# Kernel tuning notes

Hardware: AMD Instinct MI355X
Metric: run time of the kernel (lower is better)

## Reference

```python
import jax, jax.numpy as jnp
import numpy as np
from jax import lax

B = 4096
IM = 64
HID = 256          # LSTM hidden
OBS_D = 400        # obs embedding dim
SAMP_D = 16        # sample embedding dim
ADDR_D = 16        # address embedding dim
IN_D = OBS_D + SAMP_D + ADDR_D  # 432 LSTM input dim


def setup_inputs() -> dict:
    key = jax.random.key(0)
    ks = jax.random.split(key, 32)
    n = jax.random.normal
    s = 0.05
    return {
        "obs": n(ks[0], (B, IM, IM), jnp.float32),
        "program_id": jax.random.randint(ks[1], (B,), 0, 3),
        "shape_id": jax.random.randint(ks[2], (B,), 0, 2),
        "shape_id_0": jax.random.randint(ks[3], (B,), 0, 2),
        "shape_id_1": jax.random.randint(ks[4], (B,), 0, 2),
        "eps_rp": n(ks[5], (B, 2), jnp.float32),
        "eps_rp0": n(ks[6], (B, 2), jnp.float32),
        "eps_rp1": n(ks[7], (B, 2), jnp.float32),
        # CNN obs embedder (stand-in for util.init_cnn(output_dim=16), flattening to 400)
        "conv1_w": n(ks[8], (32, 1, 3, 3)) * s,
        "conv1_b": n(ks[9], (32,)) * s,
        "conv2_w": n(ks[10], (16, 32, 3, 3)) * s,
        "conv2_b": n(ks[11], (16,)) * s,
        # raw_position_embedder: MLP 2 -> 100 -> 100 -> 16
        "mlp_w1": n(ks[12], (100, 2)) * s,
        "mlp_b1": n(ks[13], (100,)) * s,
        "mlp_w2": n(ks[14], (100, 100)) * s,
        "mlp_b2": n(ks[15], (100,)) * s,
        "mlp_w3": n(ks[16], (SAMP_D, 100)) * s,
        "mlp_b3": n(ks[17], (SAMP_D,)) * s,
        # LSTMCell params (PyTorch layout: [4H, in], gate order i,f,g,o)
        "W_ih": n(ks[18], (4 * HID, IN_D)) * s,
        "b_ih": n(ks[19], (4 * HID,)) * s,
        "W_hh": n(ks[20], (4 * HID, HID)) * s,
        "b_hh": n(ks[21], (4 * HID,)) * s,
        "addr_emb": n(ks[22], (7, ADDR_D)),
        "pid_emb": n(ks[23], (3, SAMP_D)),
        "sid_emb": n(ks[24], (2, SAMP_D)),
        "pid_ext_w": n(ks[25], (3, HID)) * s,
        "pid_ext_b": n(ks[26], (3,)) * s,
        "sid_ext_w": n(ks[27], (2, HID)) * s,
        "sid_ext_b": n(ks[28], (2,)) * s,
        "rp_ext_w": n(ks[29], (4, HID)) * s,
        "rp_ext_b": n(ks[30], (4,)) * s,
    }


def reference(obs, program_id, shape_id, shape_id_0, shape_id_1, eps_rp, eps_rp0, eps_rp1,
              conv1_w, conv1_b, conv2_w, conv2_b,
              mlp_w1, mlp_b1, mlp_w2, mlp_b2, mlp_w3, mlp_b3,
              W_ih, b_ih, W_hh, b_hh,
              addr_emb, pid_emb, sid_emb,
              pid_ext_w, pid_ext_b, sid_ext_w, sid_ext_b, rp_ext_w, rp_ext_b):
    b = obs.shape[0]
    # obs embedder: [B,1,64,64] -> conv s2 -> conv s2 -> avgpool 3x3 -> [B,16,5,5] -> [B,400]
    x = obs[:, None]
    x = jax.nn.relu(lax.conv_general_dilated(x, conv1_w, (2, 2), ((1, 1), (1, 1))) + conv1_b[None, :, None, None])
    x = jax.nn.relu(lax.conv_general_dilated(x, conv2_w, (2, 2), ((1, 1), (1, 1))) + conv2_b[None, :, None, None])
    x = lax.reduce_window(x, 0.0, lax.add, (1, 1, 3, 3), (1, 1, 3, 3), 'VALID') / 9.0
    obs_emb = x.reshape(b, OBS_D)

    def step(samp, aid, h, c):
        a = jnp.broadcast_to(addr_emb[aid], (b, ADDR_D))
        xin = jnp.concatenate([obs_emb, samp, a], axis=-1)
        g = xin @ W_ih.T + b_ih + h @ W_hh.T + b_hh
        i, f, gg, o = jnp.split(g, 4, axis=-1)
        c2 = jax.nn.sigmoid(f) * c + jax.nn.sigmoid(i) * jnp.tanh(gg)
        return jax.nn.sigmoid(o) * jnp.tanh(c2), c2

    zs = jnp.zeros((b, SAMP_D), obs.dtype)
    zh = jnp.zeros((b, HID), obs.dtype)
    h0, c0 = step(zs, 0, zh, zh)
    pid_logits = h0 @ pid_ext_w.T + pid_ext_b
    prev_pid = pid_emb[program_id]

    # branch 0 (program_id == 0): shape_id then raw_position
    h1, c1 = step(prev_pid, 1, h0, c0)
    sid_logits = h1 @ sid_ext_w.T + sid_ext_b
    h2, _ = step(sid_emb[shape_id], 4, h1, c1)
    rp = h2 @ rp_ext_w.T + rp_ext_b
    rp_b0 = rp[:, :2] + jnp.exp(rp[:, 2:]) * eps_rp

    # branch 1 (program_id != 0): shape_id_0, shape_id_1, raw_position_0, raw_position_1
    h1b, c1b = step(prev_pid, 2, h0, c0)
    sid0_logits = h1b @ sid_ext_w.T + sid_ext_b
    h2b, c2b = step(sid_emb[shape_id_0], 3, h1b, c1b)
    sid1_logits = h2b @ sid_ext_w.T + sid_ext_b
    h3b, c3b = step(sid_emb[shape_id_1], 5, h2b, c2b)
    rp0p = h3b @ rp_ext_w.T + rp_ext_b
    rp0 = rp0p[:, :2] + jnp.exp(rp0p[:, 2:]) * eps_rp0
    z = jnp.tanh(rp0 @ mlp_w1.T + mlp_b1)
    z = jnp.tanh(z @ mlp_w2.T + mlp_b2)
    rp0_emb = z @ mlp_w3.T + mlp_b3
    h4b, _ = step(rp0_emb, 6, h3b, c3b)
    rp1p = h4b @ rp_ext_w.T + rp_ext_b
    rp1 = rp1p[:, :2] + jnp.exp(rp1p[:, 2:]) * eps_rp1

    # [B, 3+2+2+2+2+2+2] = [B, 15]
    return jnp.concatenate([pid_logits, sid_logits, rp_b0, sid0_logits, sid1_logits, rp0, rp1], axis=-1)
```

## Files before the change

### kernel.cpp

```cpp
#include <hip/hip_runtime.h>
#include <hip/hip_bf16.h>
#include <math.h>

#define BATCH 4096
#define HID 256
#define OUT_W 15
#define AK 448

typedef unsigned short ushort_t;
typedef unsigned int uint_t;

using bf16x8 = __attribute__((ext_vector_type(8))) short;
using f32x4v = __attribute__((ext_vector_type(4))) float;
using f32x2 = __attribute__((ext_vector_type(2))) float;

__device__ __forceinline__ float sigf(float x) { return 1.0f / (1.0f + __expf(-x)); }
__device__ __forceinline__ float tanh_fast(float x) { return 1.0f - 2.0f / (__expf(2.0f * x) + 1.0f); }
__device__ __forceinline__ float bf2f(ushort_t u) { return __uint_as_float(((uint_t)u) << 16); }
__device__ __forceinline__ ushort_t f2bf(float x) {
    uint_t b = __float_as_uint(x);
    return (ushort_t)((b + 0x7fffu + ((b >> 16) & 1u)) >> 16);
}

__global__ __launch_bounds__(256) void prep_kernel(
    const float* __restrict__ W_ih, const float* __restrict__ W_hh,
    const float* __restrict__ b_ih, const float* __restrict__ b_hh,
    const float* __restrict__ addr_emb, const float* __restrict__ pid_emb,
    const float* __restrict__ sid_emb,
    const float* __restrict__ mlp_w2, const float* __restrict__ mlp_w3,
    const float* __restrict__ conv1_w, const float* __restrict__ conv1_b,
    const float* __restrict__ conv2_w,
    float* __restrict__ W_ih_T, ushort_t* __restrict__ Wb,
    float* __restrict__ bias_all, float* __restrict__ pid_rows,
    float* __restrict__ sid_rows, float* __restrict__ w2t, float* __restrict__ w3t,
    float* __restrict__ w1pp, ushort_t* __restrict__ Btg,
    ushort_t* __restrict__ Wobs_b)
{
    int blk = blockIdx.x, t = threadIdx.x;
    if (blk < 16) {
        __shared__ float tile[64][65];
        int j0 = blk * 64;
        int k0 = 384;
        for (int i = t; i < 4096; i += 256) {
            int r = i >> 6, c = i & 63;
            int k = k0 + c;
            tile[r][c] = (k < 432) ? W_ih[(size_t)(j0 + r) * 432 + k] : 0.f;
        }
        __syncthreads();
        for (int i = t; i < 4096; i += 256) {
            int r = i >> 6, c = i & 63;
            int k = k0 + r;
            if (k < 432) W_ih_T[(size_t)k * 1024 + j0 + c] = tile[c][r];
        }
    } else if (blk == 16) {
        const int aids[7] = {0, 1, 4, 2, 3, 5, 6};
        for (int s = 0; s < 7; s++) {
            int aid = aids[s];
            for (int j = t; j < 1024; j += 256) {
                float v = b_ih[j] + b_hh[j];
                #pragma unroll
                for (int k = 0; k < 16; k++)
                    v += addr_emb[aid * 16 + k] * W_ih[(size_t)j * 432 + 416 + k];
                bias_all[s * 1024 + j] = v;
            }
        }
    } else if (blk == 17) {
        for (int p = 0; p < 3; p++)
            for (int j = t; j < 1024; j += 256) {
                float v = 0.f;
                #pragma unroll
                for (int k = 0; k < 16; k++)
                    v += pid_emb[p * 16 + k] * W_ih[(size_t)j * 432 + 400 + k];
                pid_rows[p * 1024 + j] = v;
            }
        for (int p = 0; p < 2; p++)
            for (int j = t; j < 1024; j += 256) {
                float v = 0.f;
                #pragma unroll
                for (int k = 0; k < 16; k++)
                    v += sid_emb[p * 16 + k] * W_ih[(size_t)j * 432 + 400 + k];
                sid_rows[p * 1024 + j] = v;
            }
    } else if (blk == 18) {
        for (int i = t; i < 10000; i += 256) {
            int o = i / 100, k = i % 100;
            w2t[k * 100 + o] = mlp_w2[i];
        }
        for (int i = t; i < 1600; i += 256) {
            int o = i / 100, k = i % 100;
            w3t[k * 16 + o] = mlp_w3[i];
        }
    } else if (blk == 19) {
        for (int i = t; i < 320; i += 256) {
            int half = i & 1, idx = i >> 1;
            int k = idx % 10, pr = idx / 10;
            int icq = pr >> 2, i2 = pr & 3;
            int ic = icq * 8 + i2 + half * 4;
            w1pp[i] = (k < 9) ? conv1_w[ic * 9 + k] : conv1_b[ic];
        }
        for (int i = t; i < 4608; i += 256) {
            int tap = i >> 9;
            int rem = i & 511;
            int oc = rem >> 5, ic = rem & 31;
            Btg[i] = f2bf(conv2_w[(size_t)(oc * 32 + ic) * 9 + tap]);
        }
    } else if (blk < 36) {
        int seg = blk - 20;
        for (int i = seg * 16384 + t; i < (seg + 1) * 16384; i += 256)
            Wb[i] = f2bf(W_hh[i]);
    } else {
        int col0 = (blk - 36) * 32;
        for (int i = t; i < 32 * AK; i += 256) {
            int c = col0 + i / AK, k = i % AK;
            Wobs_b[(size_t)c * AK + k] = (k < 400) ? f2bf(W_ih[(size_t)c * 432 + k]) : (ushort_t)0;
        }
    }
}

#define CE_RS 640
#define CO_RS 680
#define SM2S 72
#define C2S_CS 324
#define C2S_RS 20
__global__ __launch_bounds__(512, 4) void conv_kernel(
    const float* __restrict__ obs, const float* __restrict__ w1pp,
    const ushort_t* __restrict__ Btg, const float* __restrict__ b2,
    ushort_t* __restrict__ obs_emb_b)
{
    __shared__ __align__(16) ushort_t cE[17 * CE_RS];
    __shared__ __align__(16) ushort_t cO[17 * CO_RS];
    __shared__ __align__(16) float c2s[16 * C2S_CS];
    __shared__ __align__(16) float sm2[33 * SM2S];
    __shared__ __align__(16) float w1s[320];
    const int b = blockIdx.x, t = threadIdx.x;
    const float* og = obs + (size_t)b * 4096;

    const int w = t >> 6, L = t & 63, q = L >> 4, ln = L & 15;

    {
        uint_t* zE = (uint_t*)cE;
        uint_t* zO = (uint_t*)cO;
        for (int i = t; i < CE_RS / 2; i += 512) zE[i] = 0;
        for (int i = t; i < CO_RS / 2; i += 512) zO[i] = 0;
        if (t < 320) {
            int row = (t / 20) + 1, d = t % 20;
            zO[row * (CO_RS / 2) + d] = 0;
        }
    }
    if (t < 80) ((float4*)w1s)[t] = ((const float4*)w1pp)[t];
    if (t < 33) {
        int sw = (t >> 1) & 1;
        sm2[t * SM2S + sw * 4 + 3] = 0.f;
    }

    auto stage_obs = [&](int ph) {
        for (int i = t; i < 33 * 16; i += 512) {
            int row = i >> 4, c4 = i & 15;
            int sw = (row >> 1) & 1;
            int orow = 32 * ph - 1 + row;
            float4 v = float4{0.f, 0.f, 0.f, 0.f};
            if (orow >= 0) v = ((const float4*)(og + (size_t)orow * 64))[c4];
            *(float4*)&sm2[row * SM2S + ((1 + c4) ^ sw) * 4] = v;
        }
    };

    auto conv1_phase = [&](int ph) {
        const int r = t >> 5, g = (t >> 2) & 7, icq = t & 3;
        const int brow = ph ? r : (r + 1);
        float Pt[3][12];
        #pragma unroll
        for (int d = 0; d < 3; d++) {
            int row = 2 * r + d;
            int sw = (row >> 1) & 1;
            const float* base = &sm2[row * SM2S];
            #pragma unroll
            for (int j4 = 0; j4 < 3; j4++) {
                float4 v = *(const float4*)(base + ((2 * g + j4) ^ sw) * 4);
                Pt[d][j4 * 4 + 0] = v.x; Pt[d][j4 * 4 + 1] = v.y;
                Pt[d][j4 * 4 + 2] = v.z; Pt[d][j4 * 4 + 3] = v.w;
            }
        }
        const float* wpbase = &w1s[icq * 80];
        #pragma unroll
        for (int p = 0; p < 4; p++) {
            f32x2 pbc[9];
            #pragma unroll
            for (int d = 0; d < 3; d++)
                #pragma unroll
                for (int dx = 0; dx < 3; dx++) {
                    float v = Pt[d][2 * p + 3 + dx];
                    pbc[d * 3 + dx] = f32x2{v, v};
                }
            f32x2 sall[4];
            #pragma unroll
            for (int i = 0; i < 4; i++) {
                const float* wp = wpbase + i * 20;
                float4 wv0 = *(const float4*)(wp);
                float4 wv1 = *(const float4*)(wp + 4);
                float4 wv2 = *(const float4*)(wp + 8);
                float4 wv3 = *(const float4*)(wp + 12);
                float4 wv4 = *(const float4*)(wp + 16);
                f32x2 W2[10] = {f32x2{wv0.x, wv0.y}, f32x2{wv0.z, wv0.w},
                                f32x2{wv1.x, wv1.y}, f32x2{wv1.z, wv1.w},
                                f32x2{wv2.x, wv2.y}, f32x2{wv2.z, wv2.w},
                                f32x2{wv3.x, wv3.y}, f32x2{wv3.z, wv3.w},
                                f32x2{wv4.x, wv4.y}, f32x2{wv4.z, wv4.w}};
                f32x2 a2 = W2[9];
                #pragma unroll
                for (int k = 0; k < 9; k++)
                    a2 = __builtin_elementwise_fma(pbc[k], W2[k], a2);
                a2 = __builtin_elementwise_max(a2, f32x2{0.f, 0.f});
                sall[i] = a2;
            }
            uint_t d0, d1, d2, d3;
            asm("v_cvt_pk_bf16_f32 %0, %1, %2" : "=v"(d0) : "v"(sall[0].x), "v"(sall[1].x));
            asm("v_cvt_pk_bf16_f32 %0, %1, %2" : "=v"(d1) : "v"(sall[2].x), "v"(sall[3].x));
            asm("v_cvt_pk_bf16_f32 %0, %1, %2" : "=v"(d2) : "v"(sall[0].y), "v"(sall[1].y));
            asm("v_cvt_pk_bf16_f32 %0, %1, %2" : "=v"(d3) : "v"(sall[2].y), "v"(sall[3].y));
            int c = 4 * g + p;
            ushort_t* dst = (c & 1)
                ? &cO[brow * CO_RS + ((c + 1) >> 1) * 40 + icq * 8]
                : &cE[brow * CE_RS + (c >> 1) * 40 + icq * 8];
            *(uint4*)dst = uint4{d0, d1, d2, d3};
        }
    };

    auto conv2_phase = [&](int ph) {
        bf16x8 Bv[9];
        #pragma unroll
        for (int tap = 0; tap < 9; tap++)
            Bv[tap] = *reinterpret_cast<const bf16x8*>(&Btg[(tap * 16 + ln) * 32 + q * 8]);
        const int y = 8 * ph + w;
        f32x4v C = {0.f, 0.f, 0.f, 0.f};
        #pragma unroll
        for (int dy = 0; dy < 3; dy++) {
            int br = 2 * y + dy;
            if (br >= 17) br -= 17;
            bf16x8 a0 = *reinterpret_cast<const bf16x8*>(&cO[br * CO_RS + ln * 40 + q * 8]);
            bf16x8 a1 = *reinterpret_cast<const bf16x8*>(&cE[br * CE_RS + ln * 40 + q * 8]);
            bf16x8 a2 = *reinterpret_cast<const bf16x8*>(&cO[br * CO_RS + (ln + 1) * 40 + q * 8]);
            C = __builtin_amdgcn_mfma_f32_16x16x32_bf16(a0, Bv[dy * 3 + 0], C, 0, 0, 0);
            C = __builtin_amdgcn_mfma_f32_16x16x32_bf16(a1, Bv[dy * 3 + 1], C, 0, 0, 0);
            C = __builtin_amdgcn_mfma_f32_16x16x32_bf16(a2, Bv[dy * 3 + 2], C, 0, 0, 0);
        }
        float bb2 = b2[ln];
        float4 o;
        o.x = fmaxf(C[0] + bb2, 0.f);
        o.y = fmaxf(C[1] + bb2, 0.f);
        o.z = fmaxf(C[2] + bb2, 0.f);
        o.w = fmaxf(C[3] + bb2, 0.f);
        *(float4*)&c2s[ln * C2S_CS + y * C2S_RS + q * 4] = o;
    };

    stage_obs(0);
    __syncthreads();
    conv1_phase(0);
    __syncthreads();
    stage_obs(1);
    conv2_phase(0);
    __syncthreads();
    conv1_phase(1);
    __syncthreads();
    conv2_phase(1);
    __syncthreads();

    ushort_t* ew = (ushort_t*)w1s;
    if (t < 400) {
        int c = t / 25, rem = t % 25, py = rem / 5, px = rem % 5;
        float s = 0.f;
        #pragma unroll
        for (int dy = 0; dy < 3; dy++)
            #pragma unroll
            for (int dx = 0; dx < 3; dx++)
                s += c2s[c * C2S_CS + (3 * py + dy) * C2S_RS + 3 * px + dx];
        ew[t] = f2bf(s * (1.f / 9.f));
    } else if (t < AK) {
        ew[t] = 0;
    }
    __syncthreads();
    if (t < 56)
        ((uint4*)(obs_emb_b + (size_t)b * AK))[t] = ((const uint4*)ew)[t];
}

__global__ __launch_bounds__(256) void obs_gemm(
    const ushort_t* __restrict__ Ab, const ushort_t* __restrict__ Wob,
    ushort_t* __restrict__ outp)
{
    __shared__ __align__(16) ushort_t As[64 * 72];
    __shared__ __align__(16) ushort_t ob[64 * 132];
    const int t = threadIdx.x;
    const int bm = blockIdx.x & 63, bu = blockIdx.x >> 6;
    const int b0 = bm * 64, n0 = bu * 128;
    const int w = t >> 6, L = t & 63, q = L >> 4, ln = L & 15;
    const int m0 = w * 16;

    f32x4v acc[8];
    #pragma unroll
    for (int i = 0; i < 8; i++) acc[i] = f32x4v{0.f, 0.f, 0.f, 0.f};

    for (int kc = 0; kc < 7; kc++) {
        #pragma unroll
        for (int ii = 0; ii < 2; ii++) {
            int i = t + ii * 256;
            int row = i >> 3, c8 = i & 7;
            *(uint4*)&As[row * 72 + c8 * 8] =
                *(const uint4*)&Ab[(size_t)(b0 + row) * AK + kc * 64 + c8 * 8];
        }
        __syncthreads();
        bf16x8 a[2];
        #pragma unroll
        for (int ks = 0; ks < 2; ks++)
            a[ks] = *reinterpret_cast<const bf16x8*>(&As[(m0 + ln) * 72 + ks * 32 + q * 8]);
        #pragma unroll
        for (int ct = 0; ct < 8; ct++) {
            const ushort_t* wr = Wob + (size_t)(n0 + ct * 16 + ln) * AK + kc * 64 + q * 8;
            bf16x8 bv0 = *reinterpret_cast<const bf16x8*>(wr);
            bf16x8 bv1 = *reinterpret_cast<const bf16x8*>(wr + 32);
            acc[ct] = __builtin_amdgcn_mfma_f32_16x16x32_bf16(a[0], bv0, acc[ct], 0, 0, 0);
            acc[ct] = __builtin_amdgcn_mfma_f32_16x16x32_bf16(a[1], bv1, acc[ct], 0, 0, 0);
        }
        __syncthreads();
    }
    #pragma unroll
    for (int ct = 0; ct < 8; ct++)
        #pragma unroll
        for (int j = 0; j < 4; j++)
            ob[(m0 + q * 4 + j) * 132 + ct * 16 + ln] = f2bf(acc[ct][j]);
    __syncthreads();
    #pragma unroll
    for (int p2 = 0; p2 < 4; p2++) {
        int idx = t + p2 * 256;
        int row = idx >> 4, c8 = idx & 15;
        uint4 v = *(const uint4*)&ob[row * 132 + c8 * 8];
        *(uint4*)&outp[(size_t)(b0 + row) * 1024 + n0 + c8 * 8] = v;
    }
}

template <int N>
__device__ __forceinline__ void head_logits_f(
    const ushort_t* hsrc, const float* __restrict__ hw, const float* __restrict__ hb,
    int off, float* red, float* __restrict__ out, int b0, int t)
{
    const int row = t >> 5, seg = t & 31;
    float part[N] = {};
    const ushort_t* hr = hsrc + row * 272 + seg * 8;
    #pragma unroll
    for (int e = 0; e < 8; e++) {
        float hv = bf2f(hr[e]);
        #pragma unroll
        for (int m = 0; m < N; m++) part[m] += hv * hw[m * 256 + seg * 8 + e];
    }
    #pragma unroll
    for (int m = 0; m < N; m++) red[(row * 32 + seg) * 4 + m] = part[m];
    __syncthreads();
    if (t < 16 * N) {
        int r2 = t / N, m = t % N;
        float s = hb[m];
        for (int p = 0; p < 32; p++) s += red[(r2 * 32 + p) * 4 + m];
        out[(size_t)(b0 + r2) * OUT_W + off + m] = s;
    }
    __syncthreads();
}

__device__ __forceinline__ void head_rp_f(
    const ushort_t* hsrc, const float* __restrict__ hw, const float* __restrict__ hb,
    const float* __restrict__ eps, int off, float* red, float* hdr,
    float* __restrict__ out, float* rp0s, int b0, int t)
{
    const int row = t >> 5, seg = t & 31;
    float part[4] = {0.f, 0.f, 0.f, 0.f};
    const ushort_t* hr = hsrc + row * 272 + seg * 8;
    #pragma unroll
    for (int e = 0; e < 8; e++) {
        float hv = bf2f(hr[e]);
        #pragma unroll
        for (int m = 0; m < 4; m++) part[m] += hv * hw[m * 256 + seg * 8 + e];
    }
    #pragma unroll
    for (int m = 0; m < 4; m++) red[(row * 32 + seg) * 4 + m] = part[m];
    __syncthreads();
    if (t < 64) {
        int r2 = t >> 2, m = t & 3;
        float s = hb[m];
        for (int p = 0; p < 32; p++) s += red[(r2 * 32 + p) * 4 + m];
        hdr[t] = s;
    }
    __syncthreads();
    if (t < 16) {
        int R = b0 + t;
        float v0 = hdr[t * 4 + 0] + __expf(hdr[t * 4 + 2]) * eps[(size_t)R * 2 + 0];
        float v1 = hdr[t * 4 + 1] + __expf(hdr[t * 4 + 3]) * eps[(size_t)R * 2 + 1];
        out[(size_t)R * OUT_W + off + 0] = v0;
        out[(size_t)R * OUT_W + off + 1] = v1;
        if (rp0s) { rp0s[t * 2 + 0] = v0; rp0s[t * 2 + 1] = v1; }
    }
    __syncthreads();
}

__global__ __launch_bounds__(512, 2) void lstm_chain(
    const ushort_t* __restrict__ obs_part, const float* __restrict__ bias_all,
    const float* __restrict__ pid_rows, const float* __restrict__ sid_rows,
    const int* __restrict__ program_id, const int* __restrict__ shape_id,
    const int* __restrict__ shape_id_0, const int* __restrict__ shape_id_1,
    const ushort_t* __restrict__ Wb, const float* __restrict__ WsampT,
    const float* __restrict__ pid_ext_w, const float* __restrict__ pid_ext_b,
    const float* __restrict__ sid_ext_w, const float* __restrict__ sid_ext_b,
    const float* __restrict__ rp_ext_w, const float* __restrict__ rp_ext_b,
    const float* __restrict__ eps_rp, const float* __restrict__ eps_rp0,
    const float* __restrict__ eps_rp1,
    const float* __restrict__ mlp_w1, const float* __restrict__ mlp_b1,
    const float* __restrict__ w2t, const float* __restrict__ mlp_b2,
    const float* __restrict__ w3t, const float* __restrict__ mlp_b3,
    float* __restrict__ out)
{
    __shared__ __align__(16) ushort_t ps_t[1024 * 20];
    __shared__ __align__(16) ushort_t hbuf[3][16 * 272];
    __shared__ float red[16 * 32 * 4];
    __shared__ float hdr[64];
    __shared__ float z1s[16][104], z2s[16][104];
    __shared__ float emb_s[16][20];
    __shared__ float rp0s[16][2];
    __shared__ int sidx_s[4][16];

    const int t = threadIdx.x;
    const int b0 = blockIdx.x * 16;
    const int w = t >> 6, L = t & 63, q = L >> 4, ln = L & 15;
    const int U = w * 32;

    if (t < 64) {
        int tbl = t >> 4, r = t & 15;
        const int* src = (tbl == 0) ? program_id : (tbl == 1) ? shape_id
                       : (tbl == 2) ? shape_id_0 : shape_id_1;
        sidx_s[tbl][r] = src[b0 + r];
    }
    for (int i = t; i < 2048; i += 512) {
        int row = i >> 7, c8 = (i & 127) * 8;
        uint4 v = *(const uint4*)&obs_part[(size_t)(b0 + row) * 1024 + c8];
        uint_t dw[4] = {v.x, v.y, v.z, v.w};
        #pragma unroll
        for (int k = 0; k < 4; k++) {
            ps_t[(c8 + 2 * k) * 20 + row] = (ushort_t)(dw[k] & 0xffffu);
            ps_t[(c8 + 2 * k + 1) * 20 + row] = (ushort_t)(dw[k] >> 16);
        }
    }
    __syncthreads();

    float cA[8], cB[8];
    f32x4v acc[4][2];

    #pragma unroll
    for (int h = 0; h < 2; h++) {
        const int unit = U + h * 16 + ln;
        float pre[4][4];
        #pragma unroll
        for (int g = 0; g < 4; g++) {
            uint2 pv = *(const uint2*)&ps_t[(g * 256 + unit) * 20 + q * 4];
            float bg = bias_all[g * 256 + unit];
            pre[g][0] = bf2f((ushort_t)(pv.x & 0xffffu)) + bg;
            pre[g][1] = bf2f((ushort_t)(pv.x >> 16)) + bg;
            pre[g][2] = bf2f((ushort_t)(pv.y & 0xffffu)) + bg;
            pre[g][3] = bf2f((ushort_t)(pv.y >> 16)) + bg;
        }
        #pragma unroll
        for (int j = 0; j < 4; j++) {
            float c2 = sigf(pre[0][j]) * tanh_fast(pre[2][j]);
            float hv = sigf(pre[3][j]) * tanh_fast(c2);
            cA[j * 2 + h] = c2; cB[j * 2 + h] = c2;
            hbuf[0][(q * 4 + j) * 272 + unit] = f2bf(hv);
        }
    }
    __syncthreads();

    auto gemm = [&](int src) {
        bf16x8 a[8];
        #pragma unroll
        for (int kk = 0; kk < 8; kk++)
            a[kk] = *reinterpret_cast<const bf16x8*>(&hbuf[src][ln * 272 + kk * 32 + q * 8]);
        #pragma unroll
        for (int g = 0; g < 4; g++)
            #pragma unroll
            for (int h = 0; h < 2; h++) {
                f32x4v z = {0.f, 0.f, 0.f, 0.f};
                const ushort_t* wr = Wb + (size_t)(g * 256 + U + h * 16 + ln) * 256 + q * 8;
                #pragma unroll
                for (int kk = 0; kk < 8; kk++)
                    z = __builtin_amdgcn_mfma_f32_16x16x32_bf16(a[kk],
                        *reinterpret_cast<const bf16x8*>(wr + kk * 32), z, 0, 0, 0);
                acc[g][h] = z;
            }
    };

    auto epi = [&](int bi, const float* samp, int tbl, int dst, float* cr) {
        #pragma unroll
        for (int h = 0; h < 2; h++) {
            const int unit = U + h * 16 + ln;
            float pre[4][4];
            #pragma unroll
            for (int g = 0; g < 4; g++) {
                uint2 pv = *(const uint2*)&ps_t[(g * 256 + unit) * 20 + q * 4];
                float bg = bias_all[bi * 1024 + g * 256 + unit];
                pre[g][0] = acc[g][h][0] + bf2f((ushort_t)(pv.x & 0xffffu)) + bg;
                pre[g][1] = acc[g][h][1] + bf2f((ushort_t)(pv.x >> 16)) + bg;
                pre[g][2] = acc[g][h][2] + bf2f((ushort_t)(pv.y & 0xffffu)) + bg;
                pre[g][3] = acc[g][h][3] + bf2f((ushort_t)(pv.y >> 16)) + bg;
            }
            #pragma unroll
            for (int j = 0; j < 4; j++) {
                int si = sidx_s[tbl][q * 4 + j];
                #pragma unroll
                for (int g = 0; g < 4; g++)
                    pre[g][j] += samp[(size_t)si * 1024 + g * 256 + unit];
            }
            #pragma unroll
            for (int j = 0; j < 4; j++) {
                float ci = cr[j * 2 + h];
                float c2 = sigf(pre[1][j]) * ci + sigf(pre[0][j]) * tanh_fast(pre[2][j]);
                float hv = sigf(pre[3][j]) * tanh_fast(c2);
                cr[j * 2 + h] = c2;
                hbuf[dst][(q * 4 + j) * 272 + unit] = f2bf(hv);
            }
        }
    };

    head_logits_f<3>(hbuf[0], pid_ext_w, pid_ext_b, 0, red, out, b0, t);

    gemm(0);
    epi(1, pid_rows, 0, 1, cA);
    epi(3, pid_rows, 0, 2, cB);
    __syncthreads();

    head_logits_f<2>(hbuf[1], sid_ext_w, sid_ext_b, 3, red, out, b0, t);

    gemm(1);
    epi(2, sid_rows, 1, 0, cA);
    __syncthreads();

    head_rp_f(hbuf[0], rp_ext_w, rp_ext_b, eps_rp, 5, red, hdr, out, nullptr, b0, t);

    gemm(2);
    epi(4, sid_rows, 2, 1, cB);
    __syncthreads();

    head_logits_f<2>(hbuf[2], sid_ext_w, sid_ext_b, 7, red, out, b0, t);
    head_logits_f<2>(hbuf[1], sid_ext_w, sid_ext_b, 9, red, out, b0, t);

    gemm(1);
    epi(5, sid_rows, 3, 2, cB);
    __syncthreads();

    head_rp_f(hbuf[2], rp_ext_w, rp_ext_b, eps_rp0, 11, red, hdr, out, &rp0s[0][0], b0, t);

    for (int i = t; i < 1600; i += 512) {
        int row = i / 100, j = i % 100;
        z1s[row][j] = tanh_fast(mlp_b1[j] + mlp_w1[j * 2] * rp0s[row][0]
                                          + mlp_w1[j * 2 + 1] * rp0s[row][1]);
    }
    __syncthreads();
    for (int i = t; i < 1600; i += 512) {
        int row = i / 100, j = i % 100;
        float s = mlp_b2[j];
        for (int k = 0; k < 100; k++) s += w2t[k * 100 + j] * z1s[row][k];
        z2s[row][j] = tanh_fast(s);
    }
    __syncthreads();
    if (t < 256) {
        int row = t >> 4, o = t & 15;
        float s = mlp_b3[o];
        for (int k = 0; k < 100; k++) s += w3t[k * 16 + o] * z2s[row][k];
        emb_s[row][o] = s;
    }
    __syncthreads();

    gemm(2);
    #pragma unroll
    for (int h = 0; h < 2; h++) {
        const int unit = U + h * 16 + ln;
        float pre[4][4];
        #pragma unroll
        for (int g = 0; g < 4; g++) {
            uint2 pv = *(const uint2*)&ps_t[(g * 256 + unit) * 20 + q * 4];
            float bg = bias_all[6 * 1024 + g * 256 + unit];
            pre[g][0] = acc[g][h][0] + bf2f((ushort_t)(pv.x & 0xffffu)) + bg;
            pre[g][1] = acc[g][h][1] + bf2f((ushort_t)(pv.x >> 16)) + bg;
            pre[g][2] = acc[g][h][2] + bf2f((ushort_t)(pv.y & 0xffffu)) + bg;
            pre[g][3] = acc[g][h][3] + bf2f((ushort_t)(pv.y >> 16)) + bg;
        }
        #pragma unroll
        for (int k = 0; k < 16; k++) {
            float wv[4];
            #pragma unroll
            for (int g = 0; g < 4; g++) wv[g] = WsampT[(size_t)k * 1024 + g * 256 + unit];
            #pragma unroll
            for (int j = 0; j < 4; j++) {
                float e = emb_s[q * 4 + j][k];
                #pragma unroll
                for (int g = 0; g < 4; g++) pre[g][j] += e * wv[g];
            }
        }
        #pragma unroll
        for (int j = 0; j < 4; j++) {
            float ci = cB[j * 2 + h];
            float c2 = sigf(pre[1][j]) * ci + sigf(pre[0][j]) * tanh_fast(pre[2][j]);
            float hv = sigf(pre[3][j]) * tanh_fast(c2);
            hbuf[0][(q * 4 + j) * 272 + unit] = f2bf(hv);
        }
    }
    __syncthreads();

    head_rp_f(hbuf[0], rp_ext_w, rp_ext_b, eps_rp1, 13, red, hdr, out, nullptr, b0, t);
}

extern "C" void kernel_launch(void* const* d_in, const int* in_sizes, int n_in,
                              void* d_out, int out_size, void* d_ws, size_t ws_size,
                              hipStream_t stream)
{
    const float* obs        = (const float*)d_in[0];
    const int*   program_id = (const int*)d_in[1];
    const int*   shape_id   = (const int*)d_in[2];
    const int*   shape_id_0 = (const int*)d_in[3];
    const int*   shape_id_1 = (const int*)d_in[4];
    const float* eps_rp     = (const float*)d_in[5];
    const float* eps_rp0    = (const float*)d_in[6];
    const float* eps_rp1    = (const float*)d_in[7];
    const float* conv1_w    = (const float*)d_in[8];
    const float* conv1_b    = (const float*)d_in[9];
    const float* conv2_w    = (const float*)d_in[10];
    const float* conv2_b    = (const float*)d_in[11];
    const float* mlp_w1     = (const float*)d_in[12];
    const float* mlp_b1     = (const float*)d_in[13];
    const float* mlp_w2     = (const float*)d_in[14];
    const float* mlp_b2     = (const float*)d_in[15];
    const float* mlp_w3     = (const float*)d_in[16];
    const float* mlp_b3     = (const float*)d_in[17];
    const float* W_ih       = (const float*)d_in[18];
    const float* b_ih       = (const float*)d_in[19];
    const float* W_hh       = (const float*)d_in[20];
    const float* b_hh       = (const float*)d_in[21];
    const float* addr_emb   = (const float*)d_in[22];
    const float* pid_emb    = (const float*)d_in[23];
    const float* sid_emb    = (const float*)d_in[24];
    const float* pid_ext_w  = (const float*)d_in[25];
    const float* pid_ext_b  = (const float*)d_in[26];
    const float* sid_ext_w  = (const float*)d_in[27];
    const float* sid_ext_b  = (const float*)d_in[28];
    const float* rp_ext_w   = (const float*)d_in[29];
    const float* rp_ext_b   = (const float*)d_in[30];
    float* out = (float*)d_out;

    float* ws = (float*)d_ws;
    size_t off = 0;
    float* W_ih_T   = ws + off; off += 432 * 1024;
    ushort_t* Wb    = (ushort_t*)(ws + off); off += 131072;
    float* bias_all = ws + off; off += 7 * 1024;
    float* pid_rows = ws + off; off += 3 * 1024;
    float* sid_rows = ws + off; off += 2 * 1024;
    ushort_t* obs_emb_b = (ushort_t*)(ws + off); off += (size_t)BATCH * AK / 2;
    ushort_t* Wobs_b    = (ushort_t*)(ws + off); off += (size_t)1024 * AK / 2;
    ushort_t* obs_part = (ushort_t*)(ws + off); off += (size_t)BATCH * 512;
    float* w2t = ws + off; off += 10000;
    float* w3t = ws + off; off += 1600;
    float* w1pp = ws + off; off += 384;
    ushort_t* Btg = (ushort_t*)(ws + off); off += 2304;
    float* WsampT = W_ih_T + (size_t)400 * 1024;

    prep_kernel<<<68, 256, 0, stream>>>(W_ih, W_hh, b_ih, b_hh, addr_emb,
                                        pid_emb, sid_emb, mlp_w2, mlp_w3,
                                        conv1_w, conv1_b, conv2_w,
                                        W_ih_T, Wb, bias_all, pid_rows,
                                        sid_rows, w2t, w3t, w1pp, Btg, Wobs_b);
    conv_kernel<<<BATCH, 512, 0, stream>>>(obs, w1pp, Btg, conv2_b, obs_emb_b);
    obs_gemm<<<512, 256, 0, stream>>>(obs_emb_b, Wobs_b, obs_part);
    lstm_chain<<<256, 512, 0, stream>>>(
        obs_part, bias_all, pid_rows, sid_rows,
        program_id, shape_id, shape_id_0, shape_id_1, Wb, WsampT,
        pid_ext_w, pid_ext_b, sid_ext_w, sid_ext_b, rp_ext_w, rp_ext_b,
        eps_rp, eps_rp0, eps_rp1,
        mlp_w1, mlp_b1, w2t, mlp_b2, w3t, mlp_b3, out);
}
```

Baseline: 382.3 us.

## Halve LSTM rows per block, drop shared obs staging, batch output heads

The LSTM chain kernel now handles 8 batch rows per block instead of 16 and launches twice as many blocks with a higher occupancy hint. It stops staging the obs-part projection in shared memory and reads it directly from global in each epilogue. It also keeps all hidden states in six LDS slots so every logits and raw-position head can be computed once at the end with wave shuffles, replacing many synchronised reductions. The trade-off is that half of each MFMA tile is wasted on duplicated rows and the repeated global reads of obs_part are uncoalesced.

```diff
diff --git a/kernel.cpp b/kernel.cpp
--- a/kernel.cpp
+++ b/kernel.cpp
@@ -336,68 +336,7 @@
     }
 }
 
-template <int N>
-__device__ __forceinline__ void head_logits_f(
-    const ushort_t* hsrc, const float* __restrict__ hw, const float* __restrict__ hb,
-    int off, float* red, float* __restrict__ out, int b0, int t)
-{
-    const int row = t >> 5, seg = t & 31;
-    float part[N] = {};
-    const ushort_t* hr = hsrc + row * 272 + seg * 8;
-    #pragma unroll
-    for (int e = 0; e < 8; e++) {
-        float hv = bf2f(hr[e]);
-        #pragma unroll
-        for (int m = 0; m < N; m++) part[m] += hv * hw[m * 256 + seg * 8 + e];
-    }
-    #pragma unroll
-    for (int m = 0; m < N; m++) red[(row * 32 + seg) * 4 + m] = part[m];
-    __syncthreads();
-    if (t < 16 * N) {
-        int r2 = t / N, m = t % N;
-        float s = hb[m];
-        for (int p = 0; p < 32; p++) s += red[(r2 * 32 + p) * 4 + m];
-        out[(size_t)(b0 + r2) * OUT_W + off + m] = s;
-    }
-    __syncthreads();
-}
-
-__device__ __forceinline__ void head_rp_f(
-    const ushort_t* hsrc, const float* __restrict__ hw, const float* __restrict__ hb,
-    const float* __restrict__ eps, int off, float* red, float* hdr,
-    float* __restrict__ out, float* rp0s, int b0, int t)
-{
-    const int row = t >> 5, seg = t & 31;
-    float part[4] = {0.f, 0.f, 0.f, 0.f};
-    const ushort_t* hr = hsrc + row * 272 + seg * 8;
-    #pragma unroll
-    for (int e = 0; e < 8; e++) {
-        float hv = bf2f(hr[e]);
-        #pragma unroll
-        for (int m = 0; m < 4; m++) part[m] += hv * hw[m * 256 + seg * 8 + e];
-    }
-    #pragma unroll
-    for (int m = 0; m < 4; m++) red[(row * 32 + seg) * 4 + m] = part[m];
-    __syncthreads();
-    if (t < 64) {
-        int r2 = t >> 2, m = t & 3;
-        float s = hb[m];
-        for (int p = 0; p < 32; p++) s += red[(r2 * 32 + p) * 4 + m];
-        hdr[t] = s;
-    }
-    __syncthreads();
-    if (t < 16) {
-        int R = b0 + t;
-        float v0 = hdr[t * 4 + 0] + __expf(hdr[t * 4 + 2]) * eps[(size_t)R * 2 + 0];
-        float v1 = hdr[t * 4 + 1] + __expf(hdr[t * 4 + 3]) * eps[(size_t)R * 2 + 1];
-        out[(size_t)R * OUT_W + off + 0] = v0;
-        out[(size_t)R * OUT_W + off + 1] = v1;
-        if (rp0s) { rp0s[t * 2 + 0] = v0; rp0s[t * 2 + 1] = v1; }
-    }
-    __syncthreads();
-}
-
-__global__ __launch_bounds__(512, 2) void lstm_chain(
+__global__ __launch_bounds__(512, 4) void lstm_chain(
     const ushort_t* __restrict__ obs_part, const float* __restrict__ bias_all,
     const float* __restrict__ pid_rows, const float* __restrict__ sid_rows,
     const int* __restrict__ program_id, const int* __restrict__ shape_id,
@@ -413,60 +352,45 @@
     const float* __restrict__ w3t, const float* __restrict__ mlp_b3,
     float* __restrict__ out)
 {
-    __shared__ __align__(16) ushort_t ps_t[1024 * 20];
-    __shared__ __align__(16) ushort_t hbuf[3][16 * 272];
-    __shared__ float red[16 * 32 * 4];
-    __shared__ float hdr[64];
-    __shared__ float z1s[16][104], z2s[16][104];
-    __shared__ float emb_s[16][20];
-    __shared__ float rp0s[16][2];
-    __shared__ int sidx_s[4][16];
+    __shared__ __align__(16) ushort_t hline[6 * 8 * 272];
+    __shared__ float z1s[8][102], z2s[8][102];
+    __shared__ float emb_s[8][20];
+    __shared__ float rp0s[8][2];
+    __shared__ int sidx_s[4][8];
 
     const int t = threadIdx.x;
-    const int b0 = blockIdx.x * 16;
-    const int w = t >> 6, L = t & 63, q = L >> 4, ln = L & 15;
+    const int b0 = blockIdx.x * 8;
+    const int w = t >> 6, l = t & 63, q = l >> 4, ln = l & 15;
     const int U = w * 32;
 
-    if (t < 64) {
-        int tbl = t >> 4, r = t & 15;
+    if (t < 32) {
+        int tbl = t >> 3, r = t & 7;
         const int* src = (tbl == 0) ? program_id : (tbl == 1) ? shape_id
                        : (tbl == 2) ? shape_id_0 : shape_id_1;
         sidx_s[tbl][r] = src[b0 + r];
     }
-    for (int i = t; i < 2048; i += 512) {
-        int row = i >> 7, c8 = (i & 127) * 8;
-        uint4 v = *(const uint4*)&obs_part[(size_t)(b0 + row) * 1024 + c8];
-        uint_t dw[4] = {v.x, v.y, v.z, v.w};
-        #pragma unroll
-        for (int k = 0; k < 4; k++) {
-            ps_t[(c8 + 2 * k) * 20 + row] = (ushort_t)(dw[k] & 0xffffu);
-            ps_t[(c8 + 2 * k + 1) * 20 + row] = (ushort_t)(dw[k] >> 16);
-        }
-    }
-    __syncthreads();
 
     float cA[8], cB[8];
     f32x4v acc[4][2];
 
-    #pragma unroll
-    for (int h = 0; h < 2; h++) {
-        const int unit = U + h * 16 + ln;
-        float pre[4][4];
-        #pragma unroll
-        for (int g = 0; g < 4; g++) {
-            uint2 pv = *(const uint2*)&ps_t[(g * 256 + unit) * 20 + q * 4];
-            float bg = bias_all[g * 256 + unit];
-            pre[g][0] = bf2f((ushort_t)(pv.x & 0xffffu)) + bg;
-            pre[g][1] = bf2f((ushort_t)(pv.x >> 16)) + bg;
-            pre[g][2] = bf2f((ushort_t)(pv.y & 0xffffu)) + bg;
-            pre[g][3] = bf2f((ushort_t)(pv.y >> 16)) + bg;
-        }
-        #pragma unroll
-        for (int j = 0; j < 4; j++) {
-            float c2 = sigf(pre[0][j]) * tanh_fast(pre[2][j]);
-            float hv = sigf(pre[3][j]) * tanh_fast(c2);
-            cA[j * 2 + h] = c2; cB[j * 2 + h] = c2;
-            hbuf[0][(q * 4 + j) * 272 + unit] = f2bf(hv);
+    if (q < 2) {
+        #pragma unroll
+        for (int h = 0; h < 2; h++) {
+            const int unit = U + h * 16 + ln;
+            #pragma unroll
+            for (int j = 0; j < 4; j++) {
+                int row = q * 4 + j;
+                float pre[4];
+                #pragma unroll
+                for (int g = 0; g < 4; g++) {
+                    int col = g * 256 + unit;
+                    pre[g] = bf2f(obs_part[(size_t)(b0 + row) * 1024 + col]) + bias_all[col];
+                }
+                float c2 = sigf(pre[0]) * tanh_fast(pre[2]);
+                float hv = sigf(pre[3]) * tanh_fast(c2);
+                cA[j * 2 + h] = c2; cB[j * 2 + h] = c2;
+                hline[(0 * 8 + row) * 272 + unit] = f2bf(hv);
+            }
         }
     }
     __syncthreads();
@@ -475,7 +399,8 @@
         bf16x8 a[8];
         #pragma unroll
         for (int kk = 0; kk < 8; kk++)
-            a[kk] = *reinterpret_cast<const bf16x8*>(&hbuf[src][ln * 272 + kk * 32 + q * 8]);
+            a[kk] = *reinterpret_cast<const bf16x8*>(
+                &hline[(src * 8 + (ln & 7)) * 272 + kk * 32 + q * 8]);
         #pragma unroll
         for (int g = 0; g < 4; g++)
             #pragma unroll
@@ -491,79 +416,135 @@
     };
 
     auto epi = [&](int bi, const float* samp, int tbl, int dst, float* cr) {
-        #pragma unroll
-        for (int h = 0; h < 2; h++) {
-            const int unit = U + h * 16 + ln;
-            float pre[4][4];
-            #pragma unroll
-            for (int g = 0; g < 4; g++) {
-                uint2 pv = *(const uint2*)&ps_t[(g * 256 + unit) * 20 + q * 4];
-                float bg = bias_all[bi * 1024 + g * 256 + unit];
-                pre[g][0] = acc[g][h][0] + bf2f((ushort_t)(pv.x & 0xffffu)) + bg;
-                pre[g][1] = acc[g][h][1] + bf2f((ushort_t)(pv.x >> 16)) + bg;
-                pre[g][2] = acc[g][h][2] + bf2f((ushort_t)(pv.y & 0xffffu)) + bg;
-                pre[g][3] = acc[g][h][3] + bf2f((ushort_t)(pv.y >> 16)) + bg;
-            }
-            #pragma unroll
-            for (int j = 0; j < 4; j++) {
-                int si = sidx_s[tbl][q * 4 + j];
-                #pragma unroll
-                for (int g = 0; g < 4; g++)
-                    pre[g][j] += samp[(size_t)si * 1024 + g * 256 + unit];
-            }
-            #pragma unroll
-            for (int j = 0; j < 4; j++) {
-                float ci = cr[j * 2 + h];
-                float c2 = sigf(pre[1][j]) * ci + sigf(pre[0][j]) * tanh_fast(pre[2][j]);
-                float hv = sigf(pre[3][j]) * tanh_fast(c2);
-                cr[j * 2 + h] = c2;
-                hbuf[dst][(q * 4 + j) * 272 + unit] = f2bf(hv);
+        if (q < 2) {
+            #pragma unroll
+            for (int h = 0; h < 2; h++) {
+                const int unit = U + h * 16 + ln;
+                #pragma unroll
+                for (int j = 0; j < 4; j++) {
+                    int row = q * 4 + j;
+                    int si = sidx_s[tbl][row];
+                    float pre[4];
+                    #pragma unroll
+                    for (int g = 0; g < 4; g++) {
+                        int col = g * 256 + unit;
+                        pre[g] = acc[g][h][j]
+                               + bf2f(obs_part[(size_t)(b0 + row) * 1024 + col])
+                               + bias_all[bi * 1024 + col]
+                               + samp[(size_t)si * 1024 + col];
+                    }
+                    float c2 = sigf(pre[1]) * cr[j * 2 + h] + sigf(pre[0]) * tanh_fast(pre[2]);
+                    float hv = sigf(pre[3]) * tanh_fast(c2);
+                    cr[j * 2 + h] = c2;
+                    hline[(dst * 8 + row) * 272 + unit] = f2bf(hv);
+                }
             }
         }
     };
-
-    head_logits_f<3>(hbuf[0], pid_ext_w, pid_ext_b, 0, red, out, b0, t);
 
     gemm(0);
     epi(1, pid_rows, 0, 1, cA);
     epi(3, pid_rows, 0, 2, cB);
     __syncthreads();
 
-    head_logits_f<2>(hbuf[1], sid_ext_w, sid_ext_b, 3, red, out, b0, t);
-
     gemm(1);
-    epi(2, sid_rows, 1, 0, cA);
-    __syncthreads();
-
-    head_rp_f(hbuf[0], rp_ext_w, rp_ext_b, eps_rp, 5, red, hdr, out, nullptr, b0, t);
-
+    epi(2, sid_rows, 1, 3, cA);
     gemm(2);
-    epi(4, sid_rows, 2, 1, cB);
-    __syncthreads();
-
-    head_logits_f<2>(hbuf[2], sid_ext_w, sid_ext_b, 7, red, out, b0, t);
-    head_logits_f<2>(hbuf[1], sid_ext_w, sid_ext_b, 9, red, out, b0, t);
-
-    gemm(1);
-    epi(5, sid_rows, 3, 2, cB);
-    __syncthreads();
-
-    head_rp_f(hbuf[2], rp_ext_w, rp_ext_b, eps_rp0, 11, red, hdr, out, &rp0s[0][0], b0, t);
-
-    for (int i = t; i < 1600; i += 512) {
+    epi(4, sid_rows, 2, 4, cB);
+    __syncthreads();
+
+    gemm(4);
+    epi(5, sid_rows, 3, 5, cB);
+    __syncthreads();
+
+    {
+        const int r = w, R = b0 + r, d0 = l * 4;
+        float part[17];
+        #pragma unroll
+        for (int m = 0; m < 17; m++) part[m] = 0.f;
+        float hv[4];
+        auto ldh = [&](int src) {
+            uint2 v = *(const uint2*)&hline[(src * 8 + r) * 272 + d0];
+            hv[0] = bf2f((ushort_t)(v.x & 0xffffu)); hv[1] = bf2f((ushort_t)(v.x >> 16));
+            hv[2] = bf2f((ushort_t)(v.y & 0xffffu)); hv[3] = bf2f((ushort_t)(v.y >> 16));
+        };
+        ldh(0);
+        #pragma unroll
+        for (int m = 0; m < 3; m++) {
+            float4 wv = *(const float4*)&pid_ext_w[m * 256 + d0];
+            part[m] += hv[0] * wv.x + hv[1] * wv.y + hv[2] * wv.z + hv[3] * wv.w;
+        }
+        float4 ws0 = *(const float4*)&sid_ext_w[0 * 256 + d0];
+        float4 ws1 = *(const float4*)&sid_ext_w[1 * 256 + d0];
+        ldh(1);
+        part[3] += hv[0]*ws0.x + hv[1]*ws0.y + hv[2]*ws0.z + hv[3]*ws0.w;
+        part[4] += hv[0]*ws1.x + hv[1]*ws1.y + hv[2]*ws1.z + hv[3]*ws1.w;
+        ldh(2);
+        part[9]  += hv[0]*ws0.x + hv[1]*ws0.y + hv[2]*ws0.z + hv[3]*ws0.w;
+        part[10] += hv[0]*ws1.x + hv[1]*ws1.y + hv[2]*ws1.z + hv[3]*ws1.w;
+        ldh(4);
+        part[11] += hv[0]*ws0.x + hv[1]*ws0.y + hv[2]*ws0.z + hv[3]*ws0.w;
+        part[12] += hv[0]*ws1.x + hv[1]*ws1.y + hv[2]*ws1.z + hv[3]*ws1.w;
+        float4 wr0 = *(const float4*)&rp_ext_w[0 * 256 + d0];
+        float4 wr1 = *(const float4*)&rp_ext_w[1 * 256 + d0];
+        float4 wr2 = *(const float4*)&rp_ext_w[2 * 256 + d0];
+        float4 wr3 = *(const float4*)&rp_ext_w[3 * 256 + d0];
+        ldh(3);
+        part[5] += hv[0]*wr0.x + hv[1]*wr0.y + hv[2]*wr0.z + hv[3]*wr0.w;
+        part[6] += hv[0]*wr1.x + hv[1]*wr1.y + hv[2]*wr1.z + hv[3]*wr1.w;
+        part[7] += hv[0]*wr2.x + hv[1]*wr2.y + hv[2]*wr2.z + hv[3]*wr2.w;
+        part[8] += hv[0]*wr3.x + hv[1]*wr3.y + hv[2]*wr3.z + hv[3]*wr3.w;
+        ldh(5);
+        part[13] += hv[0]*wr0.x + hv[1]*wr0.y + hv[2]*wr0.z + hv[3]*wr0.w;
+        part[14] += hv[0]*wr1.x + hv[1]*wr1.y + hv[2]*wr1.z + hv[3]*wr1.w;
+        part[15] += hv[0]*wr2.x + hv[1]*wr2.y + hv[2]*wr2.z + hv[3]*wr2.w;
+        part[16] += hv[0]*wr3.x + hv[1]*wr3.y + hv[2]*wr3.z + hv[3]*wr3.w;
+        #pragma unroll
+        for (int m = 0; m < 17; m++) {
+            float s = part[m];
+            s += __shfl_xor(s, 1);  s += __shfl_xor(s, 2);  s += __shfl_xor(s, 4);
+            s += __shfl_xor(s, 8);  s += __shfl_xor(s, 16); s += __shfl_xor(s, 32);
+            part[m] = s;
+        }
+        if (l == 0) {
+            float* orow = out + (size_t)R * OUT_W;
+            orow[0] = part[0] + pid_ext_b[0];
+            orow[1] = part[1] + pid_ext_b[1];
+            orow[2] = part[2] + pid_ext_b[2];
+            orow[3] = part[3] + sid_ext_b[0];
+            orow[4] = part[4] + sid_ext_b[1];
+            float s0 = part[5] + rp_ext_b[0], s1 = part[6] + rp_ext_b[1];
+            float s2 = part[7] + rp_ext_b[2], s3 = part[8] + rp_ext_b[3];
+            orow[5] = s0 + __expf(s2) * eps_rp[(size_t)R * 2 + 0];
+            orow[6] = s1 + __expf(s3) * eps_rp[(size_t)R * 2 + 1];
+            orow[7] = part[9]  + sid_ext_b[0];
+            orow[8] = part[10] + sid_ext_b[1];
+            orow[9] = part[11] + sid_ext_b[0];
+            orow[10] = part[12] + sid_ext_b[1];
+            float t0 = part[13] + rp_ext_b[0], t1 = part[14] + rp_ext_b[1];
+            float t2 = part[15] + rp_ext_b[2], t3 = part[16] + rp_ext_b[3];
+            float v0 = t0 + __expf(t2) * eps_rp0[(size_t)R * 2 + 0];
+            float v1 = t1 + __expf(t3) * eps_rp0[(size_t)R * 2 + 1];
+            orow[11] = v0; orow[12] = v1;
+            rp0s[r][0] = v0; rp0s[r][1] = v1;
+        }
+    }
+    __syncthreads();
+
+    for (int i = t; i < 800; i += 512) {
         int row = i / 100, j = i % 100;
         z1s[row][j] = tanh_fast(mlp_b1[j] + mlp_w1[j * 2] * rp0s[row][0]
                                           + mlp_w1[j * 2 + 1] * rp0s[row][1]);
     }
     __syncthreads();
-    for (int i = t; i < 1600; i += 512) {
+    for (int i = t; i < 800; i += 512) {
         int row = i / 100, j = i % 100;
         float s = mlp_b2[j];
         for (int k = 0; k < 100; k++) s += w2t[k * 100 + j] * z1s[row][k];
         z2s[row][j] = tanh_fast(s);
     }
     __syncthreads();
-    if (t < 256) {
+    if (t < 128) {
         int row = t >> 4, o = t & 15;
         float s = mlp_b3[o];
         for (int k = 0; k < 100; k++) s += w3t[k * 16 + o] * z2s[row][k];
@@ -571,43 +552,69 @@
     }
     __syncthreads();
 
-    gemm(2);
-    #pragma unroll
-    for (int h = 0; h < 2; h++) {
-        const int unit = U + h * 16 + ln;
-        float pre[4][4];
-        #pragma unroll
-        for (int g = 0; g < 4; g++) {
-            uint2 pv = *(const uint2*)&ps_t[(g * 256 + unit) * 20 + q * 4];
-            float bg = bias_all[6 * 1024 + g * 256 + unit];
-            pre[g][0] = acc[g][h][0] + bf2f((ushort_t)(pv.x & 0xffffu)) + bg;
-            pre[g][1] = acc[g][h][1] + bf2f((ushort_t)(pv.x >> 16)) + bg;
-            pre[g][2] = acc[g][h][2] + bf2f((ushort_t)(pv.y & 0xffffu)) + bg;
-            pre[g][3] = acc[g][h][3] + bf2f((ushort_t)(pv.y >> 16)) + bg;
-        }
-        #pragma unroll
-        for (int k = 0; k < 16; k++) {
-            float wv[4];
-            #pragma unroll
-            for (int g = 0; g < 4; g++) wv[g] = WsampT[(size_t)k * 1024 + g * 256 + unit];
+    gemm(5);
+    if (q < 2) {
+        #pragma unroll
+        for (int h = 0; h < 2; h++) {
+            const int unit = U + h * 16 + ln;
+            float pre[4][4];
             #pragma unroll
             for (int j = 0; j < 4; j++) {
-                float e = emb_s[q * 4 + j][k];
-                #pragma unroll
-                for (int g = 0; g < 4; g++) pre[g][j] += e * wv[g];
-            }
-        }
-        #pragma unroll
-        for (int j = 0; j < 4; j++) {
-            float ci = cB[j * 2 + h];
-            float c2 = sigf(pre[1][j]) * ci + sigf(pre[0][j]) * tanh_fast(pre[2][j]);
-            float hv = sigf(pre[3][j]) * tanh_fast(c2);
-            hbuf[0][(q * 4 + j) * 272 + unit] = f2bf(hv);
-        }
-    }
-    __syncthreads();
-
-    head_rp_f(hbuf[0], rp_ext_w, rp_ext_b, eps_rp1, 13, red, hdr, out, nullptr, b0, t);
+                int row = q * 4 + j;
+                #pragma unroll
+                for (int g = 0; g < 4; g++)
+                    pre[g][j] = acc[g][h][j]
+                              + bf2f(obs_part[(size_t)(b0 + row) * 1024 + g * 256 + unit])
+                              + bias_all[6 * 1024 + g * 256 + unit];
+            }
+            #pragma unroll
+            for (int k = 0; k < 16; k++) {
+                float wv[4];
+                #pragma unroll
+                for (int g = 0; g < 4; g++) wv[g] = WsampT[(size_t)k * 1024 + g * 256 + unit];
+                #pragma unroll
+                for (int j = 0; j < 4; j++) {
+                    float e = emb_s[q * 4 + j][k];
+                    #pragma unroll
+                    for (int g = 0; g < 4; g++) pre[g][j] += e * wv[g];
+                }
+            }
+            #pragma unroll
+            for (int j = 0; j < 4; j++) {
+                float ci = cB[j * 2 + h];
+                float c2 = sigf(pre[1][j]) * ci + sigf(pre[0][j]) * tanh_fast(pre[2][j]);
+                float hv = sigf(pre[3][j]) * tanh_fast(c2);
+                hline[(0 * 8 + q * 4 + j) * 272 + unit] = f2bf(hv);
+            }
+        }
+    }
+    __syncthreads();
+
+    {
+        const int r = w, R = b0 + r, d0 = l * 4;
+        uint2 v = *(const uint2*)&hline[(0 * 8 + r) * 272 + d0];
+        float h0_ = bf2f((ushort_t)(v.x & 0xffffu)), h1_ = bf2f((ushort_t)(v.x >> 16));
+        float h2_ = bf2f((ushort_t)(v.y & 0xffffu)), h3_ = bf2f((ushort_t)(v.y >> 16));
+        float p[4];
+        #pragma unroll
+        for (int m = 0; m < 4; m++) {
+            float4 wv = *(const float4*)&rp_ext_w[m * 256 + d0];
+            p[m] = h0_ * wv.x + h1_ * wv.y + h2_ * wv.z + h3_ * wv.w;
+        }
+        #pragma unroll
+        for (int m = 0; m < 4; m++) {
+            float s = p[m];
+            s += __shfl_xor(s, 1);  s += __shfl_xor(s, 2);  s += __shfl_xor(s, 4);
+            s += __shfl_xor(s, 8);  s += __shfl_xor(s, 16); s += __shfl_xor(s, 32);
+            p[m] = s;
+        }
+        if (l == 0) {
+            float s0 = p[0] + rp_ext_b[0], s1 = p[1] + rp_ext_b[1];
+            float s2 = p[2] + rp_ext_b[2], s3 = p[3] + rp_ext_b[3];
+            out[(size_t)R * OUT_W + 13] = s0 + __expf(s2) * eps_rp1[(size_t)R * 2 + 0];
+            out[(size_t)R * OUT_W + 14] = s1 + __expf(s3) * eps_rp1[(size_t)R * 2 + 1];
+        }
+    }
 }
 
 extern "C" void kernel_launch(void* const* d_in, const int* in_sizes, int n_in,
@@ -670,7 +677,7 @@
                                         sid_rows, w2t, w3t, w1pp, Btg, Wobs_b);
     conv_kernel<<<BATCH, 512, 0, stream>>>(obs, w1pp, Btg, conv2_b, obs_emb_b);
     obs_gemm<<<512, 256, 0, stream>>>(obs_emb_b, Wobs_b, obs_part);
-    lstm_chain<<<256, 512, 0, stream>>>(
+    lstm_chain<<<512, 512, 0, stream>>>(
         obs_part, bias_all, pid_rows, sid_rows,
         program_id, shape_id, shape_id_0, shape_id_1, Wb, WsampT,
         pid_ext_w, pid_ext_b, sid_ext_w, sid_ext_b, rp_ext_w, rp_ext_b,
```

Result: slower. 513.9 us (+34.4%).
